# Kernel tuning notes

Hardware: AMD Instinct MI355X
Metric: run time of the kernel (lower is better)

Reference implementation:

```python
import jax, jax.numpy as jnp
import numpy as np

K = 5        # kernel_size
G = 1        # group_size
S = 2        # scale_factor
PAD = K // 2


def setup_inputs() -> dict:
    key = jax.random.key(0)
    k1, k2 = jax.random.split(key)
    N, C, H, W = 2, 256, 128, 128
    sH, sW = H * S, W * S
    features = jax.random.normal(k1, (N, C, H, W), dtype=jnp.float32)
    raw = jax.random.uniform(k2, (N, G * K * K, sH, sW), dtype=jnp.float32)
    # CARAFEPack softmax-normalizes masks over the k*k window per group; emulate that here
    m = raw.reshape(N, G, K * K, sH, sW)
    m = m / jnp.sum(m, axis=2, keepdims=True)
    masks = m.reshape(N, G * K * K, sH, sW)
    return {"features": features, "masks": masks}


def _carafe(features, masks):
    N, C, H, W = features.shape
    sH, sW = H * S, W * S
    Cg = C // G
    # zero-pad spatial dims so every output location has a full k x k neighborhood
    fpad = jnp.pad(features, ((0, 0), (0, 0), (PAD, PAD), (PAD, PAD)))  # [N,C,H+2p,W+2p]
    m = masks.reshape(N, G, K * K, sH, sW)
    out = jnp.zeros((N, G, Cg, sH, sW), dtype=features.dtype)
    # loop over the fixed k*k kernel offsets (25 iters): shift, nearest-upsample, weight, accumulate
    for di in range(K):
        for dj in range(K):
            shifted = fpad[:, :, di:di + H, dj:dj + W]                      # [N,C,H,W]
            up = jnp.repeat(jnp.repeat(shifted, S, axis=2), S, axis=3)      # [N,C,sH,sW] nearest upsample
            w = m[:, :, di * K + dj][:, :, None]                            # [N,G,1,sH,sW]
            out = out + up.reshape(N, G, Cg, sH, sW) * w
    return out.reshape(N, C, sH, sW)


def reference(features, masks):
    return _carafe(features, masks)
```

## Files before the change

kernel.cpp:

```cpp
#include <hip/hip_runtime.h>


namespace {
constexpr int N_ = 2, C_ = 256, H_ = 128, W_ = 128;
constexpr int K_ = 5, S_ = 2, PAD_ = 2;
constexpr int SH_ = H_ * S_, SW_ = W_ * S_;
constexpr int CPB = 16;
constexpr int TPB = 256;
constexpr int RPB = 2;
constexpr int HB_ = H_ / RPB;
constexpr int LW  = W_ + 2 * PAD_;
constexpr int LROWS = RPB + 2 * PAD_;
constexpr int LSZ = LROWS * LW;
constexpr int NSLOT = (LSZ + TPB - 1) / TPB;
typedef float v2f __attribute__((ext_vector_type(2)));
}

__global__ __launch_bounds__(TPB, 2) void carafe_kernel(
    const float* __restrict__ feat,
    const float* __restrict__ masks,
    float* __restrict__ out)
{
    __shared__ float lds[2][LSZ];

    const int bx = blockIdx.x;
    const int n  = bx / HB_;
    const int h0 = (bx % HB_) * RPB;
    const int t  = threadIdx.x;
    const int hl = t >> 7;
    const int w  = t & (W_ - 1);
    const int h  = h0 + hl;
    const int c0 = blockIdx.y * CPB;

    int  goff[NSLOT];
    bool gval[NSLOT];
#pragma unroll
    for (int s = 0; s < NSLOT; ++s) {
        int idx = s * TPB + t;
        int r  = idx / LW, cc = idx % LW;
        int gy = h0 - PAD_ + r, gx = cc - PAD_;
        bool ok = (idx < LSZ) && ((unsigned)gy < (unsigned)H_) && ((unsigned)gx < (unsigned)W_);
        gval[s] = ok;
        goff[s] = ok ? (gy * W_ + gx) : 0;
    }

    float m0[25], m1[25], m2[25], m3[25];
    {
        const float* mb = masks + ((size_t)n * 25) * (SH_ * SW_)
                                + (size_t)(S_ * h) * SW_ + S_ * w;
#pragma unroll
        for (int k = 0; k < 25; ++k) {
            v2f tt = *(const v2f*)(mb + (size_t)k * (SH_ * SW_));
            v2f bb = *(const v2f*)(mb + (size_t)k * (SH_ * SW_) + SW_);
            m0[k] = tt.x; m1[k] = tt.y; m2[k] = bb.x; m3[k] = bb.y;
        }
    }

    const float* fb = feat + ((size_t)n * C_ + c0) * (H_ * W_);
    float*       ob = out + (((size_t)n * C_ + c0) * SH_ + (size_t)(S_ * h)) * SW_ + S_ * w;

    auto issue = [&](int c, float* st) {
        const float* f = fb + (size_t)c * (H_ * W_);
#pragma unroll
        for (int s = 0; s < NSLOT; ++s) st[s] = gval[s] ? f[goff[s]] : 0.f;
    };
    auto land = [&](int b, const float* st) {
#pragma unroll
        for (int s = 0; s < NSLOT; ++s) {
            int idx = s * TPB + t;
            if (idx < LSZ) lds[b][idx] = st[s];
        }
    };
    auto compute_store = [&](const float* __restrict__ L, int c) {
        float a0 = 0.f, a1 = 0.f, a2 = 0.f, a3 = 0.f;
#pragma unroll
        for (int di = 0; di < K_; ++di) {
            const float* Lr = L + (hl + di) * LW + w;
            float f0 = Lr[0], f1 = Lr[1], f2 = Lr[2], f3 = Lr[3], f4 = Lr[4];
            const int kb = di * K_;
            a0 = fmaf(f0, m0[kb + 0], a0);
            a1 = fmaf(f0, m1[kb + 0], a1);
            a2 = fmaf(f0, m2[kb + 0], a2);
            a3 = fmaf(f0, m3[kb + 0], a3);
            a0 = fmaf(f1, m0[kb + 1], a0);
            a1 = fmaf(f1, m1[kb + 1], a1);
            a2 = fmaf(f1, m2[kb + 1], a2);
            a3 = fmaf(f1, m3[kb + 1], a3);
            a0 = fmaf(f2, m0[kb + 2], a0);
            a1 = fmaf(f2, m1[kb + 2], a1);
            a2 = fmaf(f2, m2[kb + 2], a2);
            a3 = fmaf(f2, m3[kb + 2], a3);
            a0 = fmaf(f3, m0[kb + 3], a0);
            a1 = fmaf(f3, m1[kb + 3], a1);
            a2 = fmaf(f3, m2[kb + 3], a2);
            a3 = fmaf(f3, m3[kb + 3], a3);
            a0 = fmaf(f4, m0[kb + 4], a0);
            a1 = fmaf(f4, m1[kb + 4], a1);
            a2 = fmaf(f4, m2[kb + 4], a2);
            a3 = fmaf(f4, m3[kb + 4], a3);
        }
        float* oc = ob + (size_t)c * ((size_t)SH_ * SW_);
        v2f top = {a0, a1}, bot = {a2, a3};
        __builtin_nontemporal_store(top, (v2f*)oc);
        __builtin_nontemporal_store(bot, (v2f*)(oc + SW_));
    };

    float stA[NSLOT], stB[NSLOT];
#pragma unroll
    for (int s = 0; s < NSLOT; ++s) {
        int idx = s * TPB + t;
        if (idx < LSZ) lds[0][idx] = gval[s] ? fb[goff[s]] : 0.f;
    }
    issue(1, stA);

    for (int c2 = 0; c2 < CPB; c2 += 2) {
        __syncthreads();
        if (c2 + 2 < CPB) issue(c2 + 2, stB);
        compute_store(&lds[0][0], c2);
        land(1, stA);

        __syncthreads();
        if (c2 + 3 < CPB) issue(c2 + 3, stA);
        compute_store(&lds[1][0], c2 + 1);
        if (c2 + 2 < CPB) land(0, stB);
    }
}

extern "C" void kernel_launch(void* const* d_in, const int* in_sizes, int n_in,
                              void* d_out, int out_size, void* d_ws, size_t ws_size,
                              hipStream_t stream) {
    const float* feat  = (const float*)d_in[0];
    const float* masks = (const float*)d_in[1];
    float* out = (float*)d_out;
    dim3 grid(N_ * HB_, C_ / CPB);
    carafe_kernel<<<grid, dim3(TPB), 0, stream>>>(feat, masks, out);
}
```

Baseline: 56.79 us.

## Switch to single-wave blocks tiling one row by 64 columns

Each block shrinks from 256 threads covering two full output rows to a single 64-thread wavefront covering half a row, with a 5x68 LDS halo tile. The grid grows to match, so there are four times as many blocks. The double-buffered channel pipeline is also reordered so only one channel is prefetched ahead of compute, with barriers after each land. This aims for finer-grained scheduling and cheap single-wave barriers, but it costs more halo reloads per output and shallower load prefetch.

```diff
diff --git a/kernel.cpp b/kernel.cpp
--- a/kernel.cpp
+++ b/kernel.cpp
@@ -6,13 +6,12 @@
 constexpr int K_ = 5, S_ = 2, PAD_ = 2;
 constexpr int SH_ = H_ * S_, SW_ = W_ * S_;
 constexpr int CPB = 16;
-constexpr int TPB = 256;
-constexpr int RPB = 2;
-constexpr int HB_ = H_ / RPB;
-constexpr int LW  = W_ + 2 * PAD_;
-constexpr int LROWS = RPB + 2 * PAD_;
-constexpr int LSZ = LROWS * LW;
-constexpr int NSLOT = (LSZ + TPB - 1) / TPB;
+constexpr int TPB = 64;
+constexpr int TW  = 68;
+constexpr int TR  = 5;
+constexpr int TSZ = TR * TW;
+constexpr int NSLOT = (TSZ + 63) / 64;
+constexpr int SPATIAL = N_ * H_ * (W_ / 64);
 typedef float v2f __attribute__((ext_vector_type(2)));
 }
 
@@ -21,25 +20,24 @@
     const float* __restrict__ masks,
     float* __restrict__ out)
 {
-    __shared__ float lds[2][LSZ];
+    __shared__ float lds[2][TSZ];
 
-    const int bx = blockIdx.x;
-    const int n  = bx / HB_;
-    const int h0 = (bx % HB_) * RPB;
-    const int t  = threadIdx.x;
-    const int hl = t >> 7;
-    const int w  = t & (W_ - 1);
-    const int h  = h0 + hl;
-    const int c0 = blockIdx.y * CPB;
+    const int lane = threadIdx.x;
+    const int sp   = blockIdx.x;
+    const int n    = sp >> 8;
+    const int rem  = sp & 255;
+    const int h    = rem >> 1;
+    const int wc0  = (rem & 1) << 6;
+    const int c0   = blockIdx.y * CPB;
 
     int  goff[NSLOT];
     bool gval[NSLOT];
 #pragma unroll
     for (int s = 0; s < NSLOT; ++s) {
-        int idx = s * TPB + t;
-        int r  = idx / LW, cc = idx % LW;
-        int gy = h0 - PAD_ + r, gx = cc - PAD_;
-        bool ok = (idx < LSZ) && ((unsigned)gy < (unsigned)H_) && ((unsigned)gx < (unsigned)W_);
+        int idx = s * 64 + lane;
+        int r  = idx / TW, cc = idx % TW;
+        int gy = h - PAD_ + r, gx = wc0 - PAD_ + cc;
+        bool ok = (idx < TSZ) && ((unsigned)gy < (unsigned)H_) && ((unsigned)gx < (unsigned)W_);
         gval[s] = ok;
         goff[s] = ok ? (gy * W_ + gx) : 0;
     }
@@ -47,7 +45,7 @@
     float m0[25], m1[25], m2[25], m3[25];
     {
         const float* mb = masks + ((size_t)n * 25) * (SH_ * SW_)
-                                + (size_t)(S_ * h) * SW_ + S_ * w;
+                                + (size_t)(S_ * h) * SW_ + S_ * (wc0 + lane);
 #pragma unroll
         for (int k = 0; k < 25; ++k) {
             v2f tt = *(const v2f*)(mb + (size_t)k * (SH_ * SW_));
@@ -57,25 +55,26 @@
     }
 
     const float* fb = feat + ((size_t)n * C_ + c0) * (H_ * W_);
-    float*       ob = out + (((size_t)n * C_ + c0) * SH_ + (size_t)(S_ * h)) * SW_ + S_ * w;
+    float*       ob = out + (((size_t)n * C_ + c0) * SH_ + (size_t)(S_ * h)) * SW_
+                          + S_ * (wc0 + lane);
 
     auto issue = [&](int c, float* st) {
         const float* f = fb + (size_t)c * (H_ * W_);
 #pragma unroll
         for (int s = 0; s < NSLOT; ++s) st[s] = gval[s] ? f[goff[s]] : 0.f;
     };
-    auto land = [&](int b, const float* st) {
+    auto land = [&](float* tile, const float* st) {
 #pragma unroll
         for (int s = 0; s < NSLOT; ++s) {
-            int idx = s * TPB + t;
-            if (idx < LSZ) lds[b][idx] = st[s];
+            int idx = s * 64 + lane;
+            if (idx < TSZ) tile[idx] = st[s];
         }
     };
-    auto compute_store = [&](const float* __restrict__ L, int c) {
+    auto compute_store = [&](const float* L, int c) {
         float a0 = 0.f, a1 = 0.f, a2 = 0.f, a3 = 0.f;
 #pragma unroll
         for (int di = 0; di < K_; ++di) {
-            const float* Lr = L + (hl + di) * LW + w;
+            const float* Lr = L + di * TW + lane;
             float f0 = Lr[0], f1 = Lr[1], f2 = Lr[2], f3 = Lr[3], f4 = Lr[4];
             const int kb = di * K_;
             a0 = fmaf(f0, m0[kb + 0], a0);
@@ -105,24 +104,24 @@
         __builtin_nontemporal_store(bot, (v2f*)(oc + SW_));
     };
 
-    float stA[NSLOT], stB[NSLOT];
 #pragma unroll
     for (int s = 0; s < NSLOT; ++s) {
-        int idx = s * TPB + t;
-        if (idx < LSZ) lds[0][idx] = gval[s] ? fb[goff[s]] : 0.f;
+        int idx = s * 64 + lane;
+        if (idx < TSZ) lds[0][idx] = gval[s] ? fb[goff[s]] : 0.f;
     }
-    issue(1, stA);
+    __syncthreads();
 
+    float stA[NSLOT], stB[NSLOT];
     for (int c2 = 0; c2 < CPB; c2 += 2) {
+        issue(c2 + 1, stA);
+        compute_store(&lds[0][0], c2);
+        land(&lds[1][0], stA);
         __syncthreads();
+
         if (c2 + 2 < CPB) issue(c2 + 2, stB);
-        compute_store(&lds[0][0], c2);
-        land(1, stA);
-
+        compute_store(&lds[1][0], c2 + 1);
+        if (c2 + 2 < CPB) land(&lds[0][0], stB);
         __syncthreads();
-        if (c2 + 3 < CPB) issue(c2 + 3, stA);
-        compute_store(&lds[1][0], c2 + 1);
-        if (c2 + 2 < CPB) land(0, stB);
     }
 }
 
@@ -132,6 +131,6 @@
     const float* feat  = (const float*)d_in[0];
     const float* masks = (const float*)d_in[1];
     float* out = (float*)d_out;
-    dim3 grid(N_ * HB_, C_ / CPB);
+    dim3 grid(SPATIAL, C_ / CPB);
     carafe_kernel<<<grid, dim3(TPB), 0, stream>>>(feat, masks, out);
 }
```

New measurement: 68.11 us. 1.2x slower.

## Pack mask weights as bf16 pairs to cut registers and raise occupancy

Applied to the files above, without the earlier changes.

Stores the 100 per-thread mask weights as 50 packed bf16 pairs instead of fp32, unpacking with bit ops before each FMA. This reduces register pressure so launch bounds can request 4 blocks per CU, and channels per block doubles to amortize mask loads. In exchange it adds unpack ALU ops and reduces weight precision to bf16, which may affect accuracy tolerance.

```diff
diff --git a/kernel.cpp b/kernel.cpp
--- a/kernel.cpp
+++ b/kernel.cpp
@@ -5,7 +5,7 @@
 constexpr int N_ = 2, C_ = 256, H_ = 128, W_ = 128;
 constexpr int K_ = 5, S_ = 2, PAD_ = 2;
 constexpr int SH_ = H_ * S_, SW_ = W_ * S_;
-constexpr int CPB = 16;
+constexpr int CPB = 32;
 constexpr int TPB = 256;
 constexpr int RPB = 2;
 constexpr int HB_ = H_ / RPB;
@@ -14,9 +14,20 @@
 constexpr int LSZ = LROWS * LW;
 constexpr int NSLOT = (LSZ + TPB - 1) / TPB;
 typedef float v2f __attribute__((ext_vector_type(2)));
+
+__device__ __forceinline__ unsigned pack_bf16(float hi, float lo) {
+    unsigned uh = __float_as_uint(hi), ul = __float_as_uint(lo);
+    return ((uh + 0x8000u) & 0xFFFF0000u) | ((ul + 0x8000u) >> 16);
+}
+__device__ __forceinline__ float up_hi(unsigned p) {
+    return __uint_as_float(p & 0xFFFF0000u);
+}
+__device__ __forceinline__ float up_lo(unsigned p) {
+    return __uint_as_float(p << 16);
+}
 }
 
-__global__ __launch_bounds__(TPB, 2) void carafe_kernel(
+__global__ __launch_bounds__(TPB, 4) void carafe_kernel(
     const float* __restrict__ feat,
     const float* __restrict__ masks,
     float* __restrict__ out)
@@ -44,7 +55,7 @@
         goff[s] = ok ? (gy * W_ + gx) : 0;
     }
 
-    float m0[25], m1[25], m2[25], m3[25];
+    unsigned pk01[25], pk23[25];
     {
         const float* mb = masks + ((size_t)n * 25) * (SH_ * SW_)
                                 + (size_t)(S_ * h) * SW_ + S_ * w;
@@ -52,7 +63,8 @@
         for (int k = 0; k < 25; ++k) {
             v2f tt = *(const v2f*)(mb + (size_t)k * (SH_ * SW_));
             v2f bb = *(const v2f*)(mb + (size_t)k * (SH_ * SW_) + SW_);
-            m0[k] = tt.x; m1[k] = tt.y; m2[k] = bb.x; m3[k] = bb.y;
+            pk01[k] = pack_bf16(tt.x, tt.y);
+            pk23[k] = pack_bf16(bb.x, bb.y);
         }
     }
 
@@ -78,26 +90,16 @@
             const float* Lr = L + (hl + di) * LW + w;
             float f0 = Lr[0], f1 = Lr[1], f2 = Lr[2], f3 = Lr[3], f4 = Lr[4];
             const int kb = di * K_;
-            a0 = fmaf(f0, m0[kb + 0], a0);
-            a1 = fmaf(f0, m1[kb + 0], a1);
-            a2 = fmaf(f0, m2[kb + 0], a2);
-            a3 = fmaf(f0, m3[kb + 0], a3);
-            a0 = fmaf(f1, m0[kb + 1], a0);
-            a1 = fmaf(f1, m1[kb + 1], a1);
-            a2 = fmaf(f1, m2[kb + 1], a2);
-            a3 = fmaf(f1, m3[kb + 1], a3);
-            a0 = fmaf(f2, m0[kb + 2], a0);
-            a1 = fmaf(f2, m1[kb + 2], a1);
-            a2 = fmaf(f2, m2[kb + 2], a2);
-            a3 = fmaf(f2, m3[kb + 2], a3);
-            a0 = fmaf(f3, m0[kb + 3], a0);
-            a1 = fmaf(f3, m1[kb + 3], a1);
-            a2 = fmaf(f3, m2[kb + 3], a2);
-            a3 = fmaf(f3, m3[kb + 3], a3);
-            a0 = fmaf(f4, m0[kb + 4], a0);
-            a1 = fmaf(f4, m1[kb + 4], a1);
-            a2 = fmaf(f4, m2[kb + 4], a2);
-            a3 = fmaf(f4, m3[kb + 4], a3);
+#pragma unroll
+            for (int dj = 0; dj < K_; ++dj) {
+                float f = (dj == 0) ? f0 : (dj == 1) ? f1 : (dj == 2) ? f2
+                        : (dj == 3) ? f3 : f4;
+                unsigned p01 = pk01[kb + dj], p23 = pk23[kb + dj];
+                a0 = fmaf(f, up_hi(p01), a0);
+                a1 = fmaf(f, up_lo(p01), a1);
+                a2 = fmaf(f, up_hi(p23), a2);
+                a3 = fmaf(f, up_lo(p23), a3);
+            }
         }
         float* oc = ob + (size_t)c * ((size_t)SH_ * SW_);
         v2f top = {a0, a1}, bot = {a2, a3};
```

Result: slower. 73.97 us (+30.2%).
